# Kernel tuning notes

Hardware: AMD Instinct MI355X
Metric: run time of the kernel (lower is better)

## Reference

```python
import jax, jax.numpy as jnp
import numpy as np

N = 100000   # num nodes
E = 1200000  # num edges
D = 64       # feature dim (input and both hidden layers)
R = 4        # num relations


def setup_inputs() -> dict:
    key = jax.random.key(0)
    ks = jax.random.split(key, 16)

    def p(k, shape, scale=0.05):
        return jax.random.normal(k, shape, dtype=jnp.float32) * scale

    inp = {
        "x": p(ks[0], (N, D), 1.0),
        "src": jax.random.randint(ks[1], (E,), 0, N),
        "dst": jax.random.randint(ks[2], (E,), 0, N),
        "rel": jax.random.randint(ks[3], (E,), 0, R),
    }
    i = 4
    for layer in (1, 2):
        inp[f"conv{layer}_w"] = p(ks[i], (D, R * D)); i += 1
        inp[f"conv{layer}_b"] = jnp.zeros((D,), jnp.float32)
        inp[f"conv{layer}_ws"] = p(ks[i], (D, D)); i += 1
        inp[f"conv{layer}_bs"] = jnp.zeros((D,), jnp.float32)
        inp[f"hw{layer}_pw"] = p(ks[i], (D, 2 * D)); i += 1
        inp[f"hw{layer}_pb"] = jnp.zeros((D,), jnp.float32)
        inp[f"hw{layer}_tw"] = p(ks[i], (D, 2 * D)); i += 1
        inp[f"hw{layer}_tb"] = jnp.full((D,), -2.0, jnp.float32)  # transform bias init -2
    return inp


def _rgc(x, src, dst, rel, w, b, ws, bs):
    # RelationalGraphConv: per-(node, relation) scatter-mean of source features,
    # then linear over concatenated relation slots + self-loop linear + sigmoid.
    msg = x[src]                                  # [E, D] gather
    seg = dst * R + rel                           # [E] flattened (node, relation) id
    s = jax.ops.segment_sum(msg, seg, num_segments=N * R)          # [N*R, D]
    cnt = jax.ops.segment_sum(jnp.ones((msg.shape[0], 1), msg.dtype), seg,
                              num_segments=N * R)                  # [N*R, 1]
    upd = (s / jnp.maximum(cnt, 1.0)).reshape(N, R * x.shape[1])   # [N, R*D]
    out = upd @ w.T + b + x @ ws.T + bs
    return jax.nn.sigmoid(out)


def _highway(h, prev, pw, pb, tw, tb):
    c = jnp.concatenate([h, prev], axis=1)        # [N, 2D]
    pr = jax.nn.relu(c @ pw.T + pb)
    g = jax.nn.sigmoid(c @ tw.T + tb)
    return g * pr + (1.0 - g) * h


def reference(x, src, dst, rel,
              conv1_w, conv1_b, conv1_ws, conv1_bs,
              hw1_pw, hw1_pb, hw1_tw, hw1_tb,
              conv2_w, conv2_b, conv2_ws, conv2_bs,
              hw2_pw, hw2_pb, hw2_tw, hw2_tb):
    h1 = _rgc(x, src, dst, rel, conv1_w, conv1_b, conv1_ws, conv1_bs)
    g1 = _highway(h1, x, hw1_pw, hw1_pb, hw1_tw, hw1_tb)   # prev_gcn = input
    h2 = _rgc(g1, src, dst, rel, conv2_w, conv2_b, conv2_ws, conv2_bs)
    g2 = _highway(h2, h1, hw2_pw, hw2_pb, hw2_tw, hw2_tb)  # prev_gcn = h1 (conv1 output)
    return g2  # node_feature, [N, D]
```

## Files before the change

kernel.cpp:

```cpp
#include <hip/hip_runtime.h>

#define NN 100000
#define NE 1200000
#define NRR 400000
#define NBIN 98
#define SSZ2 384

typedef float f32x4 __attribute__((ext_vector_type(4)));
typedef __bf16 bf16x4 __attribute__((ext_vector_type(4)));
typedef __bf16 bf16x8 __attribute__((ext_vector_type(8)));

__device__ __forceinline__ float sigmoidf_(float x){ return 1.0f/(1.0f+__expf(-x)); }

__global__ __launch_bounds__(256)
void binhist_kernel(const int* __restrict__ dst, const int* __restrict__ rel,
                    int* __restrict__ bincnt){
  __shared__ int h[NBIN];
  int t = threadIdx.x;
  if (t < NBIN) h[t] = 0;
  __syncthreads();
  for (int e = blockIdx.x*256 + t; e < NE; e += 64*256){
    int bin = (dst[e]*4 + rel[e]) >> 12;
    atomicAdd(&h[bin], 1);
  }
  __syncthreads();
  if (t < NBIN && h[t]) atomicAdd(&bincnt[t], h[t]);
}

__global__ void binscan_kernel(const int* __restrict__ bincnt, int* __restrict__ binoff,
                               int* __restrict__ bincur, int* __restrict__ soff){
  if (threadIdx.x == 0){
    int s = 0;
    for (int i = 0; i < NBIN; ++i){ binoff[i] = s; bincur[i] = s; s += bincnt[i]; }
    binoff[NBIN] = NE;
    soff[NRR] = NE;
  }
}

__global__ __launch_bounds__(256)
void passA_kernel(const int* __restrict__ src, const int* __restrict__ dst,
                  const int* __restrict__ rel, int* __restrict__ bincur,
                  unsigned* __restrict__ ebin){
  __shared__ int h[NBIN], runbase[NBIN];
  int t = threadIdx.x;
  if (t < NBIN) h[t] = 0;
  __syncthreads();
  int lo = blockIdx.x*8192, hi = min(lo + 8192, NE);
  for (int e = lo + t; e < hi; e += 256)
    atomicAdd(&h[(dst[e]*4 + rel[e]) >> 12], 1);
  __syncthreads();
  if (t < NBIN){
    runbase[t] = h[t] ? atomicAdd(&bincur[t], h[t]) : 0;
    h[t] = 0;
  }
  __syncthreads();
  for (int e = lo + t; e < hi; e += 256){
    int seg = dst[e]*4 + rel[e];
    int bin = seg >> 12;
    int p = runbase[bin] + atomicAdd(&h[bin], 1);
    ebin[p] = (unsigned)src[e] | ((unsigned)(seg & 4095) << 17);
  }
}

__global__ __launch_bounds__(1024)
void passB_kernel(const unsigned* __restrict__ ebin, const int* __restrict__ binoff,
                  int* __restrict__ soff, unsigned* __restrict__ ebuck){
  __shared__ int st[4096];
  __shared__ int wsum[16], wbase[16];
  const int bin = blockIdx.x;
  const int t = threadIdx.x;
  const int base = binoff[bin], end = binoff[bin+1];
  #pragma unroll
  for (int i = 0; i < 4; ++i) st[t*4 + i] = 0;
  __syncthreads();
  for (int e = base + t; e < end; e += 1024)
    atomicAdd(&st[(ebin[e] >> 17) & 4095], 1);
  __syncthreads();
  int h0 = st[t*4], h1 = st[t*4+1], h2 = st[t*4+2], h3 = st[t*4+3];
  int lsum = h0 + h1 + h2 + h3;
  int lane = t & 63, wv = t >> 6;
  int inc = lsum;
  #pragma unroll
  for (int o = 1; o < 64; o <<= 1){ int u = __shfl_up(inc, o); if (lane >= o) inc += u; }
  if (lane == 63) wsum[wv] = inc;
  __syncthreads();
  if (t == 0){ int s = 0; for (int i = 0; i < 16; ++i){ wbase[i] = s; s += wsum[i]; } }
  __syncthreads();
  int ex = base + wbase[wv] + (inc - lsum);
  int s0 = ex, s1 = ex + h0, s2 = s1 + h1, s3 = s2 + h2;
  st[t*4] = s0; st[t*4+1] = s1; st[t*4+2] = s2; st[t*4+3] = s3;
  int sg = bin*4096 + t*4;
  if (sg   < NRR) soff[sg]   = s0;
  if (sg+1 < NRR) soff[sg+1] = s1;
  if (sg+2 < NRR) soff[sg+2] = s2;
  if (sg+3 < NRR) soff[sg+3] = s3;
  __syncthreads();
  for (int e = base + t; e < end; e += 1024){
    unsigned u = ebin[e];
    int p = atomicAdd(&st[(u >> 17) & 4095], 1);
    ebuck[p] = u & 0x1FFFFu;
  }
}

__global__ void tobf16_kernel(const float* __restrict__ xf, __bf16* __restrict__ xb){
  int i = (blockIdx.x*256 + threadIdx.x)*8;
  if (i < NN*64){
    f32x4 a = *(const f32x4*)(xf + i);
    f32x4 b = *(const f32x4*)(xf + i + 4);
    bf16x8 r;
    r[0]=(__bf16)a[0]; r[1]=(__bf16)a[1]; r[2]=(__bf16)a[2]; r[3]=(__bf16)a[3];
    r[4]=(__bf16)b[0]; r[5]=(__bf16)b[1]; r[6]=(__bf16)b[2]; r[7]=(__bf16)b[3];
    *(bf16x8*)(xb + i) = r;
  }
}

__global__ void prep_kernel(const float* __restrict__ w,  const float* __restrict__ b,
                            const float* __restrict__ ws, const float* __restrict__ bs,
                            const float* __restrict__ pw, const float* __restrict__ pb,
                            const float* __restrict__ tw, const float* __restrict__ tb,
                            __bf16* __restrict__ W1, __bf16* __restrict__ W2,
                            float* __restrict__ bias1, float* __restrict__ bias2){
  int i = blockIdx.x*256 + threadIdx.x;
  if (i < 64*320) {
    int n = i/320, k = i - n*320;
    float v = (k < 256) ? w[n*256+k] : ws[n*64 + (k-256)];
    W1[i] = (__bf16)v;
  }
  if (i < 128*128) {
    int n = i >> 7, k = i & 127;
    float v = (n < 64) ? pw[n*128+k] : tw[(n-64)*128+k];
    W2[i] = (__bf16)v;
  }
  if (i < 64)  bias1[i] = b[i] + bs[i];
  if (i < 128) bias2[i] = (i < 64) ? pb[i] : tb[i-64];
}

__global__ __launch_bounds__(256)
void gather_kernel(const unsigned* __restrict__ ebuck, const int* __restrict__ soff,
                   const __bf16* __restrict__ inb, __bf16* __restrict__ segb){
  __shared__ int sof[33];
  __shared__ int ssrc[SSZ2];
  const int b = blockIdx.x;
  const int t = threadIdx.x;
  if (t < 33) sof[t] = soff[b*32 + t];
  __syncthreads();
  const int e0 = sof[0], e1 = sof[32];
  for (int e = e0 + t; e < e1; e += 256){
    int o = e - e0;
    if (o < SSZ2) ssrc[o] = (int)ebuck[e];
  }
  __syncthreads();

  const int fl = t & 7;
  const int g  = t >> 3;
  int o0 = sof[g] - e0;
  int c  = sof[g+1] - sof[g];
  if (o0 + c > SSZ2) c = max(0, SSZ2 - o0);

  f32x4 a0 = {0.f,0.f,0.f,0.f}, a1 = {0.f,0.f,0.f,0.f};
  f32x4 b0 = {0.f,0.f,0.f,0.f}, b1 = {0.f,0.f,0.f,0.f};
  int i = 0;
  for (; i + 2 <= c; i += 2){
    int s0 = ssrc[o0+i], s1 = ssrc[o0+i+1];
    bf16x8 v0 = *(const bf16x8*)(&inb[(size_t)s0*64 + fl*8]);
    bf16x8 v1 = *(const bf16x8*)(&inb[(size_t)s1*64 + fl*8]);
    a0[0]+=(float)v0[0]; a0[1]+=(float)v0[1]; a0[2]+=(float)v0[2]; a0[3]+=(float)v0[3];
    a1[0]+=(float)v0[4]; a1[1]+=(float)v0[5]; a1[2]+=(float)v0[6]; a1[3]+=(float)v0[7];
    b0[0]+=(float)v1[0]; b0[1]+=(float)v1[1]; b0[2]+=(float)v1[2]; b0[3]+=(float)v1[3];
    b1[0]+=(float)v1[4]; b1[1]+=(float)v1[5]; b1[2]+=(float)v1[6]; b1[3]+=(float)v1[7];
  }
  if (i < c){
    int s0 = ssrc[o0+i];
    bf16x8 v0 = *(const bf16x8*)(&inb[(size_t)s0*64 + fl*8]);
    a0[0]+=(float)v0[0]; a0[1]+=(float)v0[1]; a0[2]+=(float)v0[2]; a0[3]+=(float)v0[3];
    a1[0]+=(float)v0[4]; a1[1]+=(float)v0[5]; a1[2]+=(float)v0[6]; a1[3]+=(float)v0[7];
  }
  float inv = 1.0f / fmaxf((float)c, 1.0f);
  bf16x8 r;
  r[0]=(__bf16)((a0[0]+b0[0])*inv); r[1]=(__bf16)((a0[1]+b0[1])*inv);
  r[2]=(__bf16)((a0[2]+b0[2])*inv); r[3]=(__bf16)((a0[3]+b0[3])*inv);
  r[4]=(__bf16)((a1[0]+b1[0])*inv); r[5]=(__bf16)((a1[1]+b1[1])*inv);
  r[6]=(__bf16)((a1[2]+b1[2])*inv); r[7]=(__bf16)((a1[3]+b1[3])*inv);
  *(bf16x8*)(&segb[(size_t)(b*32 + g)*64 + fl*8]) = r;
}

#define W2P 136
#define HSP 72

template<bool LAYER1>
__global__ __launch_bounds__(256)
void dense_kernel(const __bf16* __restrict__ segb,
                  const __bf16* __restrict__ xinb,
                  const __bf16* __restrict__ prevb,
                  const __bf16* __restrict__ W1,
                  const __bf16* __restrict__ W2,
                  const float* __restrict__ bias1,
                  const float* __restrict__ bias2,
                  __bf16* __restrict__ hb,
                  __bf16* __restrict__ gb,
                  float* __restrict__ outp)
{
  __shared__ __bf16 w2s[128*W2P];
  __shared__ __bf16 hs[128*HSP];

  const int tid = threadIdx.x;
  #pragma unroll
  for (int i = 0; i < 8; ++i) {
    int idx = i*2048 + tid*8;
    int n = idx >> 7, k = idx & 127;
    *(bf16x8*)(&w2s[n*W2P + k]) = *(const bf16x8*)(&W2[idx]);
  }
  __syncthreads();

  const int lane = tid & 63;
  const int wv   = tid >> 6;
  const int mloc = lane & 15;
  const int kg   = lane >> 4;
  const int base = blockIdx.x * 128;

  int arow[2];
  arow[0] = min(base      + wv*16 + mloc, NN-1);
  arow[1] = min(base + 64 + wv*16 + mloc, NN-1);

  f32x4 acc1[2][4] = {};

  #pragma unroll
  for (int kb = 0; kb < 256; kb += 32) {
    bf16x8 bf[4];
    #pragma unroll
    for (int j = 0; j < 4; ++j)
      bf[j] = *(const bf16x8*)(&W1[(j*16 + mloc)*320 + kb + kg*8]);
    #pragma unroll
    for (int h = 0; h < 2; ++h) {
      bf16x8 af = *(const bf16x8*)(&segb[(size_t)arow[h]*256 + kb + kg*8]);
      #pragma unroll
      for (int j = 0; j < 4; ++j)
        acc1[h][j] = __builtin_amdgcn_mfma_f32_16x16x32_bf16(af, bf[j], acc1[h][j], 0,0,0);
    }
  }
  #pragma unroll
  for (int kb = 0; kb < 64; kb += 32) {
    bf16x8 bf[4];
    #pragma unroll
    for (int j = 0; j < 4; ++j)
      bf[j] = *(const bf16x8*)(&W1[(j*16 + mloc)*320 + 256 + kb + kg*8]);
    #pragma unroll
    for (int h = 0; h < 2; ++h) {
      bf16x8 af = *(const bf16x8*)(&xinb[(size_t)arow[h]*64 + kb + kg*8]);
      #pragma unroll
      for (int j = 0; j < 4; ++j)
        acc1[h][j] = __builtin_amdgcn_mfma_f32_16x16x32_bf16(af, bf[j], acc1[h][j], 0,0,0);
    }
  }

  #pragma unroll
  for (int h = 0; h < 2; ++h) {
    #pragma unroll
    for (int j = 0; j < 4; ++j) {
      int col = j*16 + mloc;
      float b1 = bias1[col];
      #pragma unroll
      for (int r = 0; r < 4; ++r) {
        float hv = sigmoidf_(acc1[h][j][r] + b1);
        acc1[h][j][r] = hv;
        int trow = h*64 + wv*16 + kg*4 + r;
        hs[trow*HSP + col] = (__bf16)hv;
        if (LAYER1) {
          int grow = base + trow;
          if (grow < NN) hb[(size_t)grow*64 + col] = (__bf16)hv;
        }
      }
    }
  }

  f32x4 acc2[2][8] = {};
  #pragma unroll
  for (int kb = 0; kb < 64; kb += 32) {
    bf16x8 af[2];
    #pragma unroll
    for (int h = 0; h < 2; ++h) {
      int trow = h*64 + wv*16 + mloc;
      af[h] = *(const bf16x8*)(&hs[trow*HSP + kb + kg*8]);
    }
    #pragma unroll
    for (int j = 0; j < 8; ++j) {
      bf16x8 bf = *(const bf16x8*)(&w2s[(j*16 + mloc)*W2P + kb + kg*8]);
      #pragma unroll
      for (int h = 0; h < 2; ++h)
        acc2[h][j] = __builtin_amdgcn_mfma_f32_16x16x32_bf16(af[h], bf, acc2[h][j], 0,0,0);
    }
  }
  #pragma unroll
  for (int kb = 0; kb < 64; kb += 32) {
    bf16x8 af[2];
    #pragma unroll
    for (int h = 0; h < 2; ++h)
      af[h] = *(const bf16x8*)(&prevb[(size_t)arow[h]*64 + kb + kg*8]);
    #pragma unroll
    for (int j = 0; j < 8; ++j) {
      bf16x8 bf = *(const bf16x8*)(&w2s[(j*16 + mloc)*W2P + 64 + kb + kg*8]);
      #pragma unroll
      for (int h = 0; h < 2; ++h)
        acc2[h][j] = __builtin_amdgcn_mfma_f32_16x16x32_bf16(af[h], bf, acc2[h][j], 0,0,0);
    }
  }

  #pragma unroll
  for (int h = 0; h < 2; ++h) {
    #pragma unroll
    for (int j = 0; j < 4; ++j) {
      int col = j*16 + mloc;
      float bp = bias2[col];
      float bt = bias2[64 + col];
      #pragma unroll
      for (int r = 0; r < 4; ++r) {
        float pr = fmaxf(acc2[h][j][r] + bp, 0.0f);
        float g  = sigmoidf_(acc2[h][j+4][r] + bt);
        float hv = acc1[h][j][r];
        float ov = g*pr + (1.0f - g)*hv;
        int grow = base + h*64 + wv*16 + kg*4 + r;
        if (grow < NN) {
          if (LAYER1) gb[(size_t)grow*64 + col] = (__bf16)ov;
          else        outp[(size_t)grow*64 + col] = ov;
        }
      }
    }
  }
}

extern "C" void kernel_launch(void* const* d_in, const int* in_sizes, int n_in,
                              void* d_out, int out_size, void* d_ws, size_t ws_size,
                              hipStream_t stream){
  const float* x    = (const float*)d_in[0];
  const int*   src  = (const int*)d_in[1];
  const int*   dst  = (const int*)d_in[2];
  const int*   rel  = (const int*)d_in[3];
  const float* c1w  = (const float*)d_in[4];
  const float* c1b  = (const float*)d_in[5];
  const float* c1ws = (const float*)d_in[6];
  const float* c1bs = (const float*)d_in[7];
  const float* h1pw = (const float*)d_in[8];
  const float* h1pb = (const float*)d_in[9];
  const float* h1tw = (const float*)d_in[10];
  const float* h1tb = (const float*)d_in[11];
  const float* c2w  = (const float*)d_in[12];
  const float* c2b  = (const float*)d_in[13];
  const float* c2ws = (const float*)d_in[14];
  const float* c2bs = (const float*)d_in[15];
  const float* h2pw = (const float*)d_in[16];
  const float* h2pb = (const float*)d_in[17];
  const float* h2tw = (const float*)d_in[18];
  const float* h2tb = (const float*)d_in[19];

  char* p = (char*)d_ws;
  __bf16* segb = (__bf16*)p;  p += (size_t)NRR*64*2;
  __bf16* xb   = (__bf16*)p;  p += (size_t)NN*64*2;
  __bf16* h1b  = (__bf16*)p;  p += (size_t)NN*64*2;
  __bf16* g1b  = (__bf16*)p;  p += (size_t)NN*64*2;
  unsigned* ebuck = (unsigned*)p; p += (size_t)NE*4;
  unsigned* ebin  = (unsigned*)p; p += (size_t)NE*4;
  int* soff    = (int*)p;     p += (size_t)(NRR+8)*4;
  int* bincnt  = (int*)p;     p += 128*4;
  int* binoff  = (int*)p;     p += 128*4;
  int* bincur  = (int*)p;     p += 128*4;
  __bf16* W1a  = (__bf16*)p;  p += 64*320*2;
  __bf16* W2a  = (__bf16*)p;  p += 128*128*2;
  __bf16* W1b  = (__bf16*)p;  p += 64*320*2;
  __bf16* W2b  = (__bf16*)p;  p += 128*128*2;
  float* B1a   = (float*)p;   p += 64*4;
  float* B2a   = (float*)p;   p += 128*4;
  float* B1b   = (float*)p;   p += 64*4;
  float* B2b   = (float*)p;   p += 128*4;

  float* out = (float*)d_out;

  hipMemsetAsync(bincnt, 0, 128*4, stream);
  binhist_kernel<<<64, 256, 0, stream>>>(dst, rel, bincnt);
  binscan_kernel<<<1, 64, 0, stream>>>(bincnt, binoff, bincur, soff);
  passA_kernel<<<(NE+8191)/8192, 256, 0, stream>>>(src, dst, rel, bincur, ebin);
  passB_kernel<<<NBIN, 1024, 0, stream>>>(ebin, binoff, soff, ebuck);

  tobf16_kernel<<<(NN*64/8 + 255)/256, 256, 0, stream>>>(x, xb);
  prep_kernel<<<80, 256, 0, stream>>>(c1w, c1b, c1ws, c1bs, h1pw, h1pb, h1tw, h1tb,
                                      W1a, W2a, B1a, B2a);
  prep_kernel<<<80, 256, 0, stream>>>(c2w, c2b, c2ws, c2bs, h2pw, h2pb, h2tw, h2tb,
                                      W1b, W2b, B1b, B2b);

  gather_kernel<<<NRR/32, 256, 0, stream>>>(ebuck, soff, xb, segb);
  dense_kernel<true><<<(NN+127)/128, 256, 0, stream>>>(segb, xb, xb, W1a, W2a, B1a, B2a,
                                                       h1b, g1b, nullptr);
  gather_kernel<<<NRR/32, 256, 0, stream>>>(ebuck, soff, g1b, segb);
  dense_kernel<false><<<(NN+127)/128, 256, 0, stream>>>(segb, g1b, h1b, W1b, W2b, B1b, B2b,
                                                        nullptr, nullptr, out);
}
```

Before: 356.5 us.

## Shrink dense tile to 64 rows, drop W2 LDS staging, coalesce bf16 stores

The fused dense kernel now handles 64 rows per block instead of 128, with one 16-row tile per wave. It reads W2 directly from global/L2 instead of first copying it into shared memory, and adds a launch-bounds occupancy hint. Layer-1 outputs h and g are staged through LDS so they can be written as 16-byte row vectors instead of scattered 2-byte stores. The aim is less LDS and register pressure, more resident waves and blocks, and better store coalescing. In exchange, each weight fragment is reused over fewer rows, so weight reads from cache go up.

Result: slower. 417.3 us (+17.0%).

```diff
diff --git a/kernel.cpp b/kernel.cpp
--- a/kernel.cpp
+++ b/kernel.cpp
@@ -184,11 +184,10 @@
   *(bf16x8*)(&segb[(size_t)(b*32 + g)*64 + fl*8]) = r;
 }
 
-#define W2P 136
 #define HSP 72
 
 template<bool LAYER1>
-__global__ __launch_bounds__(256)
+__global__ __launch_bounds__(256, 6)
 void dense_kernel(const __bf16* __restrict__ segb,
                   const __bf16* __restrict__ xinb,
                   const __bf16* __restrict__ prevb,
@@ -200,130 +199,107 @@
                   __bf16* __restrict__ gb,
                   float* __restrict__ outp)
 {
-  __shared__ __bf16 w2s[128*W2P];
-  __shared__ __bf16 hs[128*HSP];
-
-  const int tid = threadIdx.x;
-  #pragma unroll
-  for (int i = 0; i < 8; ++i) {
-    int idx = i*2048 + tid*8;
-    int n = idx >> 7, k = idx & 127;
-    *(bf16x8*)(&w2s[n*W2P + k]) = *(const bf16x8*)(&W2[idx]);
-  }
-  __syncthreads();
-
+  __shared__ __align__(16) __bf16 hs[64*HSP];
+
+  const int tid  = threadIdx.x;
   const int lane = tid & 63;
   const int wv   = tid >> 6;
   const int mloc = lane & 15;
   const int kg   = lane >> 4;
-  const int base = blockIdx.x * 128;
-
-  int arow[2];
-  arow[0] = min(base      + wv*16 + mloc, NN-1);
-  arow[1] = min(base + 64 + wv*16 + mloc, NN-1);
-
-  f32x4 acc1[2][4] = {};
+  const int wb   = blockIdx.x*64 + wv*16;
+  const int arow = min(wb + mloc, NN-1);
+
+  f32x4 acc1[4] = {};
 
   #pragma unroll
   for (int kb = 0; kb < 256; kb += 32) {
-    bf16x8 bf[4];
-    #pragma unroll
-    for (int j = 0; j < 4; ++j)
-      bf[j] = *(const bf16x8*)(&W1[(j*16 + mloc)*320 + kb + kg*8]);
-    #pragma unroll
-    for (int h = 0; h < 2; ++h) {
-      bf16x8 af = *(const bf16x8*)(&segb[(size_t)arow[h]*256 + kb + kg*8]);
-      #pragma unroll
-      for (int j = 0; j < 4; ++j)
-        acc1[h][j] = __builtin_amdgcn_mfma_f32_16x16x32_bf16(af, bf[j], acc1[h][j], 0,0,0);
+    bf16x8 af = *(const bf16x8*)(&segb[(size_t)arow*256 + kb + kg*8]);
+    #pragma unroll
+    for (int j = 0; j < 4; ++j) {
+      bf16x8 bf = *(const bf16x8*)(&W1[(j*16 + mloc)*320 + kb + kg*8]);
+      acc1[j] = __builtin_amdgcn_mfma_f32_16x16x32_bf16(af, bf, acc1[j], 0,0,0);
     }
   }
   #pragma unroll
   for (int kb = 0; kb < 64; kb += 32) {
-    bf16x8 bf[4];
-    #pragma unroll
-    for (int j = 0; j < 4; ++j)
-      bf[j] = *(const bf16x8*)(&W1[(j*16 + mloc)*320 + 256 + kb + kg*8]);
-    #pragma unroll
-    for (int h = 0; h < 2; ++h) {
-      bf16x8 af = *(const bf16x8*)(&xinb[(size_t)arow[h]*64 + kb + kg*8]);
-      #pragma unroll
-      for (int j = 0; j < 4; ++j)
-        acc1[h][j] = __builtin_amdgcn_mfma_f32_16x16x32_bf16(af, bf[j], acc1[h][j], 0,0,0);
-    }
-  }
-
-  #pragma unroll
-  for (int h = 0; h < 2; ++h) {
+    bf16x8 af = *(const bf16x8*)(&xinb[(size_t)arow*64 + kb + kg*8]);
     #pragma unroll
     for (int j = 0; j < 4; ++j) {
-      int col = j*16 + mloc;
-      float b1 = bias1[col];
-      #pragma unroll
-      for (int r = 0; r < 4; ++r) {
-        float hv = sigmoidf_(acc1[h][j][r] + b1);
-        acc1[h][j][r] = hv;
-        int trow = h*64 + wv*16 + kg*4 + r;
-        hs[trow*HSP + col] = (__bf16)hv;
-        if (LAYER1) {
-          int grow = base + trow;
-          if (grow < NN) hb[(size_t)grow*64 + col] = (__bf16)hv;
-        }
+      bf16x8 bf = *(const bf16x8*)(&W1[(j*16 + mloc)*320 + 256 + kb + kg*8]);
+      acc1[j] = __builtin_amdgcn_mfma_f32_16x16x32_bf16(af, bf, acc1[j], 0,0,0);
+    }
+  }
+
+  #pragma unroll
+  for (int j = 0; j < 4; ++j) {
+    int col = j*16 + mloc;
+    float b1 = bias1[col];
+    #pragma unroll
+    for (int r = 0; r < 4; ++r) {
+      float hv = sigmoidf_(acc1[j][r] + b1);
+      acc1[j][r] = hv;
+      hs[(wv*16 + kg*4 + r)*HSP + col] = (__bf16)hv;
+    }
+  }
+
+  if (LAYER1) {
+    #pragma unroll
+    for (int i = 0; i < 2; ++i) {
+      int r2 = i*8 + (lane >> 3);
+      int c2 = lane & 7;
+      bf16x8 v = *(const bf16x8*)(&hs[(wv*16 + r2)*HSP + c2*8]);
+      int grow = wb + r2;
+      if (grow < NN) *(bf16x8*)(&hb[(size_t)grow*64 + c2*8]) = v;
+    }
+  }
+
+  f32x4 acc2[8] = {};
+  #pragma unroll
+  for (int kb = 0; kb < 64; kb += 32) {
+    bf16x8 af = *(const bf16x8*)(&hs[(wv*16 + mloc)*HSP + kb + kg*8]);
+    #pragma unroll
+    for (int j = 0; j < 8; ++j) {
+      bf16x8 bf = *(const bf16x8*)(&W2[(j*16 + mloc)*128 + kb + kg*8]);
+      acc2[j] = __builtin_amdgcn_mfma_f32_16x16x32_bf16(af, bf, acc2[j], 0,0,0);
+    }
+  }
+  #pragma unroll
+  for (int kb = 0; kb < 64; kb += 32) {
+    bf16x8 af = *(const bf16x8*)(&prevb[(size_t)arow*64 + kb + kg*8]);
+    #pragma unroll
+    for (int j = 0; j < 8; ++j) {
+      bf16x8 bf = *(const bf16x8*)(&W2[(j*16 + mloc)*128 + 64 + kb + kg*8]);
+      acc2[j] = __builtin_amdgcn_mfma_f32_16x16x32_bf16(af, bf, acc2[j], 0,0,0);
+    }
+  }
+
+  #pragma unroll
+  for (int j = 0; j < 4; ++j) {
+    int col = j*16 + mloc;
+    float bp = bias2[col];
+    float bt = bias2[64 + col];
+    #pragma unroll
+    for (int r = 0; r < 4; ++r) {
+      float pr = fmaxf(acc2[j][r] + bp, 0.0f);
+      float g  = sigmoidf_(acc2[j+4][r] + bt);
+      float hv = acc1[j][r];
+      float ov = g*pr + (1.0f - g)*hv;
+      if (LAYER1) {
+        hs[(wv*16 + kg*4 + r)*HSP + col] = (__bf16)ov;
+      } else {
+        int grow = wb + kg*4 + r;
+        if (grow < NN) outp[(size_t)grow*64 + col] = ov;
       }
     }
   }
-
-  f32x4 acc2[2][8] = {};
-  #pragma unroll
-  for (int kb = 0; kb < 64; kb += 32) {
-    bf16x8 af[2];
-    #pragma unroll
-    for (int h = 0; h < 2; ++h) {
-      int trow = h*64 + wv*16 + mloc;
-      af[h] = *(const bf16x8*)(&hs[trow*HSP + kb + kg*8]);
-    }
-    #pragma unroll
-    for (int j = 0; j < 8; ++j) {
-      bf16x8 bf = *(const bf16x8*)(&w2s[(j*16 + mloc)*W2P + kb + kg*8]);
-      #pragma unroll
-      for (int h = 0; h < 2; ++h)
-        acc2[h][j] = __builtin_amdgcn_mfma_f32_16x16x32_bf16(af[h], bf, acc2[h][j], 0,0,0);
-    }
-  }
-  #pragma unroll
-  for (int kb = 0; kb < 64; kb += 32) {
-    bf16x8 af[2];
-    #pragma unroll
-    for (int h = 0; h < 2; ++h)
-      af[h] = *(const bf16x8*)(&prevb[(size_t)arow[h]*64 + kb + kg*8]);
-    #pragma unroll
-    for (int j = 0; j < 8; ++j) {
-      bf16x8 bf = *(const bf16x8*)(&w2s[(j*16 + mloc)*W2P + 64 + kb + kg*8]);
-      #pragma unroll
-      for (int h = 0; h < 2; ++h)
-        acc2[h][j] = __builtin_amdgcn_mfma_f32_16x16x32_bf16(af[h], bf, acc2[h][j], 0,0,0);
-    }
-  }
-
-  #pragma unroll
-  for (int h = 0; h < 2; ++h) {
-    #pragma unroll
-    for (int j = 0; j < 4; ++j) {
-      int col = j*16 + mloc;
-      float bp = bias2[col];
-      float bt = bias2[64 + col];
-      #pragma unroll
-      for (int r = 0; r < 4; ++r) {
-        float pr = fmaxf(acc2[h][j][r] + bp, 0.0f);
-        float g  = sigmoidf_(acc2[h][j+4][r] + bt);
-        float hv = acc1[h][j][r];
-        float ov = g*pr + (1.0f - g)*hv;
-        int grow = base + h*64 + wv*16 + kg*4 + r;
-        if (grow < NN) {
-          if (LAYER1) gb[(size_t)grow*64 + col] = (__bf16)ov;
-          else        outp[(size_t)grow*64 + col] = ov;
-        }
-      }
+  if (LAYER1) {
+    #pragma unroll
+    for (int i = 0; i < 2; ++i) {
+      int r2 = i*8 + (lane >> 3);
+      int c2 = lane & 7;
+      bf16x8 v = *(const bf16x8*)(&hs[(wv*16 + r2)*HSP + c2*8]);
+      int grow = wb + r2;
+      if (grow < NN) *(bf16x8*)(&gb[(size_t)grow*64 + c2*8]) = v;
     }
   }
 }
@@ -387,9 +363,9 @@
                                       W1b, W2b, B1b, B2b);
 
   gather_kernel<<<NRR/32, 256, 0, stream>>>(ebuck, soff, xb, segb);
-  dense_kernel<true><<<(NN+127)/128, 256, 0, stream>>>(segb, xb, xb, W1a, W2a, B1a, B2a,
-                                                       h1b, g1b, nullptr);
+  dense_kernel<true><<<(NN+63)/64, 256, 0, stream>>>(segb, xb, xb, W1a, W2a, B1a, B2a,
+                                                     h1b, g1b, nullptr);
   gather_kernel<<<NRR/32, 256, 0, stream>>>(ebuck, soff, g1b, segb);
-  dense_kernel<false><<<(NN+127)/128, 256, 0, stream>>>(segb, g1b, h1b, W1b, W2b, B1b, B2b,
-                                                        nullptr, nullptr, out);
-}
+  dense_kernel<false><<<(NN+63)/64, 256, 0, stream>>>(segb, g1b, h1b, W1b, W2b, B1b, B2b,
+                                                      nullptr, nullptr, out);
+}
```
